# Kernel tuning notes

Hardware: AMD Instinct MI355X
Metric: run time of the kernel (lower is better)

Reference implementation:

```python
import jax, jax.numpy as jnp
import numpy as np

D = 256          # d_embed
KD = 256         # key_d_embed
NHEAD = 8
DK = D // NHEAD  # 32
QH = QW = 128
QWS = 16
KH = KW = 64
KWS = 8
R = QWS // KWS   # qk_ratio = 2
SCALE = 1.0 / np.sqrt(DK)


def _rel_index():
    # query coords on fine grid, key coords scaled up by ratio R
    qc = np.stack(np.meshgrid(np.arange(QWS), np.arange(QWS), indexing='ij'), -1).reshape(-1, 2)
    kc = np.stack(np.meshgrid(np.arange(KWS), np.arange(KWS), indexing='ij'), -1).reshape(-1, 2) * R
    rel = qc[:, None, :] - kc[None, :, :] + (QWS - R)  # values in [0, 2*QWS-R-1]
    return jnp.asarray(rel[..., 0] * (2 * QWS - R) + rel[..., 1])  # (QWS^2, KWS^2)


def _partition(t, ws):
    # (B, h, H, W, d) -> (B, h, H/ws, W/ws, ws*ws, d)
    B, h, H, W, d = t.shape
    t = t.reshape(B, h, H // ws, ws, W // ws, ws, d).transpose(0, 1, 2, 4, 3, 5, 6)
    return t.reshape(B, h, H // ws, W // ws, ws * ws, d)


def _merge(t, ws, H, W):
    # inverse of _partition
    B, h, nH, nW, _, d = t.shape
    t = t.reshape(B, h, nH, nW, ws, ws, d).transpose(0, 1, 2, 4, 3, 5, 6)
    return t.reshape(B, h, H, W, d)


def setup_inputs() -> dict:
    key = jax.random.key(0)
    ks = jax.random.split(key, 9)
    x = jax.random.normal(ks[0], (8, QH, QW, D), dtype=jnp.float32)
    z = jax.random.normal(ks[1], (8, KH, KW, KD), dtype=jnp.float32)
    mask = jax.random.randint(ks[2], (1, NHEAD, QH // QWS, QW // QWS, QWS * QWS, KWS * KWS), 0, 2) == 1
    Wq = jax.random.normal(ks[3], (D, D), dtype=jnp.float32) * 0.02
    bq = jnp.zeros((D,), dtype=jnp.float32)
    Wkv = jax.random.normal(ks[4], (KD, 2 * D), dtype=jnp.float32) * 0.02
    bkv = jnp.zeros((2 * D,), dtype=jnp.float32)
    Wo = jax.random.normal(ks[5], (D, D), dtype=jnp.float32) * 0.02
    bo = jnp.zeros((D,), dtype=jnp.float32)
    rel_table = jax.random.normal(ks[6], ((2 * QWS - R) ** 2, NHEAD), dtype=jnp.float32) * 0.02
    return {"x": x, "z": z, "mask": mask, "Wq": Wq, "bq": bq, "Wkv": Wkv, "bkv": bkv, "Wo": Wo, "bo": bo, "rel_table": rel_table}


def reference(x, z, mask, Wq, bq, Wkv, bkv, Wo, bo, rel_table):
    B, H, W, _ = x.shape
    q = (x @ Wq + bq).reshape(B, H, W, NHEAD, DK).transpose(0, 3, 1, 2, 4)        # (B,h,H,W,dk)
    kv = (z @ Wkv + bkv).reshape(B, KH, KW, 2, NHEAD, DK).transpose(3, 0, 4, 1, 2, 5)
    k, v = kv[0], kv[1]                                                           # (B,h,_H,_W,dk)
    sq, sk = QWS // 2, KWS // 2
    q = jnp.roll(q, (-sq, -sq), axis=(2, 3))
    k = jnp.roll(k, (-sk, -sk), axis=(2, 3))
    v = jnp.roll(v, (-sk, -sk), axis=(2, 3))
    q = _partition(q, QWS)   # (B,h,nh,nw,QWS^2,dk)
    k = _partition(k, KWS)   # (B,h,nh,nw,KWS^2,dk)
    v = _partition(v, KWS)
    attn = jnp.einsum('bhnmqd,bhnmkd->bhnmqk', q, k) * SCALE
    bias = rel_table[_rel_index()].transpose(2, 0, 1)[None, :, None, None]        # (1,h,1,1,QWS^2,KWS^2)
    attn = attn + bias
    attn = jnp.where(mask, jnp.float32(-1e9), attn)
    attn = jax.nn.softmax(attn, axis=-1)
    out = jnp.einsum('bhnmqk,bhnmkd->bhnmqd', attn, v)
    out = _merge(out, QWS, H, W)
    out = jnp.roll(out, (sq, sq), axis=(2, 3))
    out = out.transpose(0, 2, 3, 1, 4).reshape(B, H, W, D)
    return out @ Wo + bo
```

## Files before the change

kernel.cpp:

```cpp
#include <hip/hip_runtime.h>
#include <hip/hip_bf16.h>
#include <type_traits>


typedef __attribute__((ext_vector_type(8))) short short8v;
typedef __attribute__((ext_vector_type(4))) float f32x4;
typedef __attribute__((ext_vector_type(8))) unsigned short ushort8v;
typedef __attribute__((ext_vector_type(4))) unsigned short ushort4v;

#define DEV __device__ __forceinline__

DEV unsigned short f2bf(float f) {
    union { float f; unsigned u; } v; v.f = f;
    unsigned r = v.u + 0x7FFFu + ((v.u >> 16) & 1u);
    return (unsigned short)(r >> 16);
}

#define ATT_SCALE 0.17677669529663687f

__global__ void prep_weights(const float* __restrict__ Wq, const float* __restrict__ Wkv,
                             const float* __restrict__ Wo,
                             unsigned short* __restrict__ WqT, unsigned short* __restrict__ WkvT,
                             unsigned short* __restrict__ WoT) {
    int idx = blockIdx.x * 256 + threadIdx.x;
    if (idx < 65536) {
        int n = idx >> 8, k = idx & 255;
        WqT[idx] = f2bf(Wq[k * 256 + n] * ATT_SCALE);
    } else if (idx < 196608) {
        int i = idx - 65536;
        int n = i >> 8, k = i & 255;
        WkvT[i] = f2bf(Wkv[k * 512 + n]);
    } else {
        int i = idx - 196608;
        int n = i >> 8, k = i & 255;
        WoT[i] = f2bf(Wo[k * 256 + n]);
    }
}

__global__ void prep_bias(const float* __restrict__ rel_table, const float* __restrict__ bq,
                          float* __restrict__ biasb, float* __restrict__ bqs) {
    int idx = blockIdx.x * 256 + threadIdx.x;
    if (idx < 131072) {
        int head = idx >> 14;
        int q = (idx >> 6) & 255;
        int k = idx & 63;
        int qi = q >> 4, qj = q & 15;
        int ki = k >> 3, kj = k & 7;
        int r0 = qi - 2 * ki + 14, r1 = qj - 2 * kj + 14;
        biasb[idx] = rel_table[(r0 * 30 + r1) * 8 + head];
    } else if (idx < 131328) {
        int i = idx - 131072;
        bqs[i] = bq[i] * ATT_SCALE;
    }
}

__global__ void prep_mask(const int* __restrict__ mask, unsigned long long* __restrict__ mp) {
    int idx = blockIdx.x * 256 + threadIdx.x;
    const int4* src = reinterpret_cast<const int4*>(mask + (size_t)idx * 64);
    unsigned long long bits = 0;
#pragma unroll
    for (int c = 0; c < 16; ++c) {
        int4 v = src[c];
        if (v.x) bits |= 1ull << (c * 4 + 0);
        if (v.y) bits |= 1ull << (c * 4 + 1);
        if (v.z) bits |= 1ull << (c * 4 + 2);
        if (v.w) bits |= 1ull << (c * 4 + 3);
    }
    mp[idx] = bits;
}

template <typename InT, bool OUT_BF16>
__global__ __launch_bounds__(256) void gemm_proj(
    const InT* __restrict__ A, const unsigned short* __restrict__ BT,
    const float* __restrict__ bias, void* __restrict__ Cout,
    int M, int N, int K)
{
    __shared__ __align__(16) unsigned short As[128][40];
    __shared__ __align__(16) unsigned short Bs[128][40];

    const int tid = threadIdx.x;
    const int mb = blockIdx.y * 128;
    const int nb = blockIdx.x * 128;
    const int w = tid >> 6, lane = tid & 63, lr = lane & 15, lg = lane >> 4;
    const int wm = (w >> 1) * 64, wn = (w & 1) * 64;

    f32x4 acc[4][4];
#pragma unroll
    for (int i = 0; i < 4; ++i)
#pragma unroll
        for (int j = 0; j < 4; ++j) acc[i][j] = {0.f, 0.f, 0.f, 0.f};

    for (int kb = 0; kb < K; kb += 32) {
        if constexpr (std::is_same<InT, float>::value) {
#pragma unroll
            for (int i = 0; i < 4; ++i) {
                int row = (tid >> 3) + i * 32;
                int c4 = (tid & 7) * 4;
                const float4 v = *reinterpret_cast<const float4*>(
                    &A[(size_t)(mb + row) * K + kb + c4]);
                ushort4v u = { f2bf(v.x), f2bf(v.y), f2bf(v.z), f2bf(v.w) };
                *reinterpret_cast<ushort4v*>(&As[row][c4]) = u;
            }
        } else {
#pragma unroll
            for (int i = 0; i < 2; ++i) {
                int flat = tid + i * 256;
                int row = flat >> 2, c8 = (flat & 3) * 8;
                ushort8v v = *reinterpret_cast<const ushort8v*>(
                    &A[(size_t)(mb + row) * K + kb + c8]);
                *reinterpret_cast<ushort8v*>(&As[row][c8]) = v;
            }
        }
#pragma unroll
        for (int i = 0; i < 2; ++i) {
            int flat = tid + i * 256;
            int row = flat >> 2, c8 = (flat & 3) * 8;
            ushort8v v = *reinterpret_cast<const ushort8v*>(
                &BT[(size_t)(nb + row) * K + kb + c8]);
            *reinterpret_cast<ushort8v*>(&Bs[row][c8]) = v;
        }
        __syncthreads();

        short8v af[4], bfr[4];
#pragma unroll
        for (int mt = 0; mt < 4; ++mt)
            af[mt] = *reinterpret_cast<const short8v*>(&As[wm + mt * 16 + lr][lg * 8]);
#pragma unroll
        for (int nt = 0; nt < 4; ++nt)
            bfr[nt] = *reinterpret_cast<const short8v*>(&Bs[wn + nt * 16 + lr][lg * 8]);
#pragma unroll
        for (int mt = 0; mt < 4; ++mt)
#pragma unroll
            for (int nt = 0; nt < 4; ++nt)
                acc[mt][nt] = __builtin_amdgcn_mfma_f32_16x16x32_bf16(
                    af[mt], bfr[nt], acc[mt][nt], 0, 0, 0);
        __syncthreads();
    }

#pragma unroll
    for (int mt = 0; mt < 4; ++mt)
#pragma unroll
        for (int nt = 0; nt < 4; ++nt)
#pragma unroll
            for (int j = 0; j < 4; ++j) {
                int row = mb + wm + mt * 16 + lg * 4 + j;
                int col = nb + wn + nt * 16 + lr;
                float v = acc[mt][nt][j] + bias[col];
                if constexpr (OUT_BF16)
                    ((unsigned short*)Cout)[(size_t)row * N + col] = f2bf(v);
                else
                    ((float*)Cout)[(size_t)row * N + col] = v;
            }
}

__global__ __launch_bounds__(256) void win_attn(
    unsigned short* __restrict__ Qbuf,
    const unsigned short* __restrict__ KVbuf,
    const unsigned long long* __restrict__ maskp,
    const float* __restrict__ biasb)
{
    __shared__ __align__(16) unsigned char Pb[256 * 128];
    __shared__ __align__(16) unsigned short Vt[32][72];

    const int tid = threadIdx.x;
    const int win = blockIdx.x, head = blockIdx.y, b = blockIdx.z;
    const int wi = win >> 3, wj = win & 7;
    const int w = tid >> 6, lane = tid & 63, lr = lane & 15, lg = lane >> 4;
    const int qb = w * 64;

    {
        int key = tid & 63, c = tid >> 6;
        int kr = (wi * 8 + (key >> 3) + 4) & 63;
        int kc = (wj * 8 + (key & 7) + 4) & 63;
        ushort8v v = *reinterpret_cast<const ushort8v*>(
            KVbuf + ((size_t)(b * 4096 + kr * 64 + kc)) * 512 + 256 + head * 32 + c * 8);
#pragma unroll
        for (int e = 0; e < 8; ++e) Vt[c * 8 + e][key] = v[e];
    }

    short8v qf[4], kf[4];
#pragma unroll
    for (int mt = 0; mt < 4; ++mt) {
        int q = qb + mt * 16 + lr;
        int gr = (wi * 16 + (q >> 4) + 8) & 127;
        int gc = (wj * 16 + (q & 15) + 8) & 127;
        qf[mt] = *reinterpret_cast<const short8v*>(
            Qbuf + ((size_t)(b * 16384 + gr * 128 + gc)) * 256 + head * 32 + lg * 8);
    }
#pragma unroll
    for (int nt = 0; nt < 4; ++nt) {
        int key = nt * 16 + lr;
        int kr = (wi * 8 + (key >> 3) + 4) & 63;
        int kc = (wj * 8 + (key & 7) + 4) & 63;
        kf[nt] = *reinterpret_cast<const short8v*>(
            KVbuf + ((size_t)(b * 4096 + kr * 64 + kc)) * 512 + head * 32 + lg * 8);
    }

    f32x4 s[4][4];
#pragma unroll
    for (int mt = 0; mt < 4; ++mt)
#pragma unroll
        for (int nt = 0; nt < 4; ++nt) s[mt][nt] = {0.f, 0.f, 0.f, 0.f};
    __builtin_amdgcn_s_setprio(1);
#pragma unroll
    for (int mt = 0; mt < 4; ++mt)
#pragma unroll
        for (int nt = 0; nt < 4; ++nt)
            s[mt][nt] = __builtin_amdgcn_mfma_f32_16x16x32_bf16(qf[mt], kf[nt], s[mt][nt], 0, 0, 0);
    __builtin_amdgcn_s_setprio(0);

    const unsigned long long* mrow = maskp + (size_t)(head * 64 + win) * 256;
#pragma unroll
    for (int mt = 0; mt < 4; ++mt) {
#pragma unroll
        for (int j = 0; j < 4; ++j) {
            int q = qb + mt * 16 + lg * 4 + j;
            unsigned long long mb = mrow[q];
            const float* brow = biasb + (size_t)(head * 256 + q) * 64;
            float v[4];
            float m = -3.0e38f;
#pragma unroll
            for (int nt = 0; nt < 4; ++nt) {
                int key = nt * 16 + lr;
                float sv = s[mt][nt][j] + brow[key];
                if ((mb >> key) & 1ull) sv = -1.0e9f;
                v[nt] = sv;
                m = fmaxf(m, sv);
            }
#pragma unroll
            for (int d = 1; d < 16; d <<= 1) m = fmaxf(m, __shfl_xor(m, d, 64));
            float sum = 0.f;
#pragma unroll
            for (int nt = 0; nt < 4; ++nt) { v[nt] = __expf(v[nt] - m); sum += v[nt]; }
#pragma unroll
            for (int d = 1; d < 16; d <<= 1) sum += __shfl_xor(sum, d, 64);
            float inv = 1.0f / sum;
            int sw = (q & 7) << 4;
#pragma unroll
            for (int nt = 0; nt < 4; ++nt) {
                int off = q * 128 + (((nt * 16 + lr) * 2) ^ sw);
                *reinterpret_cast<unsigned short*>(Pb + off) = f2bf(v[nt] * inv);
            }
        }
    }

    __syncthreads();

    f32x4 o[4][2];
#pragma unroll
    for (int mt = 0; mt < 4; ++mt)
#pragma unroll
        for (int nt = 0; nt < 2; ++nt) o[mt][nt] = {0.f, 0.f, 0.f, 0.f};
#pragma unroll
    for (int kc = 0; kc < 2; ++kc) {
        short8v pf[4], vf[2];
#pragma unroll
        for (int mt = 0; mt < 4; ++mt) {
            int row = qb + mt * 16 + lr;
            int coff = (kc * 64 + lg * 16) ^ ((row & 7) << 4);
            pf[mt] = *reinterpret_cast<const short8v*>(Pb + row * 128 + coff);
        }
#pragma unroll
        for (int nt = 0; nt < 2; ++nt)
            vf[nt] = *reinterpret_cast<const short8v*>(&Vt[nt * 16 + lr][kc * 32 + lg * 8]);
        __builtin_amdgcn_s_setprio(1);
#pragma unroll
        for (int mt = 0; mt < 4; ++mt)
#pragma unroll
            for (int nt = 0; nt < 2; ++nt)
                o[mt][nt] = __builtin_amdgcn_mfma_f32_16x16x32_bf16(pf[mt], vf[nt], o[mt][nt], 0, 0, 0);
        __builtin_amdgcn_s_setprio(0);
    }

#pragma unroll
    for (int mt = 0; mt < 4; ++mt)
#pragma unroll
        for (int j = 0; j < 4; ++j) {
            int q = qb + mt * 16 + lg * 4 + j;
            int gr = (wi * 16 + (q >> 4) + 8) & 127;
            int gc = (wj * 16 + (q & 15) + 8) & 127;
            unsigned short* dst =
                Qbuf + ((size_t)(b * 16384 + gr * 128 + gc)) * 256 + head * 32;
#pragma unroll
            for (int nt = 0; nt < 2; ++nt)
                dst[nt * 16 + lr] = f2bf(o[mt][nt][j]);
        }
}

extern "C" void kernel_launch(void* const* d_in, const int* in_sizes, int n_in,
                              void* d_out, int out_size, void* d_ws, size_t ws_size,
                              hipStream_t stream) {
    const float* x    = (const float*)d_in[0];
    const float* z    = (const float*)d_in[1];
    const int*   mask = (const int*)d_in[2];
    const float* Wq   = (const float*)d_in[3];
    const float* bq   = (const float*)d_in[4];
    const float* Wkv  = (const float*)d_in[5];
    const float* bkv  = (const float*)d_in[6];
    const float* Wo   = (const float*)d_in[7];
    const float* bo   = (const float*)d_in[8];
    const float* rel  = (const float*)d_in[9];
    float* out = (float*)d_out;

    char* ws = (char*)d_ws;
    unsigned short*     Qbuf  = (unsigned short*)(ws);
    unsigned short*     KVbuf = (unsigned short*)(ws + 67108864);
    unsigned short*     WqT   = (unsigned short*)(ws + 100663296);
    unsigned short*     WkvT  = (unsigned short*)(ws + 100794368);
    unsigned short*     WoT   = (unsigned short*)(ws + 101056512);
    float*              biasb = (float*)(ws + 101187584);
    unsigned long long* maskp = (unsigned long long*)(ws + 101711872);
    float*              bqs   = (float*)(ws + 102760448);

    prep_weights<<<1024, 256, 0, stream>>>(Wq, Wkv, Wo, WqT, WkvT, WoT);
    prep_bias<<<513, 256, 0, stream>>>(rel, bq, biasb, bqs);
    prep_mask<<<512, 256, 0, stream>>>(mask, maskp);

    gemm_proj<float, true><<<dim3(2, 1024), 256, 0, stream>>>(
        x, WqT, bqs, (void*)Qbuf, 131072, 256, 256);
    gemm_proj<float, true><<<dim3(4, 256), 256, 0, stream>>>(
        z, WkvT, bkv, (void*)KVbuf, 32768, 512, 256);
    win_attn<<<dim3(64, 8, 8), 256, 0, stream>>>(Qbuf, KVbuf, maskp, biasb);
    gemm_proj<unsigned short, false><<<dim3(2, 1024), 256, 0, stream>>>(
        Qbuf, WoT, bo, (void*)out, 131072, 256, 256);
}
```

Measured before the change: 222.1 us.

## Double-buffer projection GEMM with direct global-to-LDS loads and swizzled LDS

Rewrites the projection GEMM main loop to double-buffer LDS tiles, prefetching the next K-slice while MFMAs run on the current one. Bf16 operands are staged with global_load_lds direct copies, while fp32 inputs are prefetched into registers and converted after the MFMAs. The padded LDS layout is replaced by an XOR-swizzled 64-byte row layout to avoid bank conflicts. The aim is to hide global memory latency and remove a barrier per iteration, at the cost of doubled LDS use and more register pressure.

```diff
diff --git a/kernel.cpp b/kernel.cpp
--- a/kernel.cpp
+++ b/kernel.cpp
@@ -69,72 +69,109 @@
     mp[idx] = bits;
 }
 
-template <typename InT, bool OUT_BF16>
+template <bool AF32, bool OUT_BF16>
 __global__ __launch_bounds__(256) void gemm_proj(
-    const InT* __restrict__ A, const unsigned short* __restrict__ BT,
+    const void* __restrict__ Ain, const unsigned short* __restrict__ BT,
     const float* __restrict__ bias, void* __restrict__ Cout,
     int M, int N, int K)
 {
-    __shared__ __align__(16) unsigned short As[128][40];
-    __shared__ __align__(16) unsigned short Bs[128][40];
+    __shared__ __align__(16) unsigned char As[2][8192];
+    __shared__ __align__(16) unsigned char Bs[2][8192];
+    const float* Af = (const float*)Ain;
+    const unsigned short* Ab = (const unsigned short*)Ain;
 
     const int tid = threadIdx.x;
-    const int mb = blockIdx.y * 128;
-    const int nb = blockIdx.x * 128;
+    const int mb = blockIdx.y * 128, nb = blockIdx.x * 128;
     const int w = tid >> 6, lane = tid & 63, lr = lane & 15, lg = lane >> 4;
     const int wm = (w >> 1) * 64, wn = (w & 1) * 64;
 
+    const int cr0 = (w << 5) + (lane >> 2);
+    const int csp = lane & 3;
+    const int cs0 = csp ^ ((cr0 >> 1) & 3);
+    const int cs1 = csp ^ (((cr0 + 16) >> 1) & 3);
+
+    auto stageB = [&](int buf, int kb) {
+        __builtin_amdgcn_global_load_lds(
+            (const __attribute__((address_space(1))) void*)(BT + (size_t)(nb + cr0) * K + kb + cs0 * 8),
+            (__attribute__((address_space(3))) void*)(&Bs[buf][w << 11]), 16, 0, 0);
+        __builtin_amdgcn_global_load_lds(
+            (const __attribute__((address_space(1))) void*)(BT + (size_t)(nb + cr0 + 16) * K + kb + cs1 * 8),
+            (__attribute__((address_space(3))) void*)(&Bs[buf][(w << 11) + 1024]), 16, 0, 0);
+    };
+    auto stageA_lds = [&](int buf, int kb) {
+        __builtin_amdgcn_global_load_lds(
+            (const __attribute__((address_space(1))) void*)(Ab + (size_t)(mb + cr0) * K + kb + cs0 * 8),
+            (__attribute__((address_space(3))) void*)(&As[buf][w << 11]), 16, 0, 0);
+        __builtin_amdgcn_global_load_lds(
+            (const __attribute__((address_space(1))) void*)(Ab + (size_t)(mb + cr0 + 16) * K + kb + cs1 * 8),
+            (__attribute__((address_space(3))) void*)(&As[buf][(w << 11) + 1024]), 16, 0, 0);
+    };
+
+    float4 areg[2][2];
+    auto loadA = [&](int kb) {
+#pragma unroll
+        for (int i = 0; i < 2; ++i) {
+            int flat = tid + (i << 8);
+            int r = flat >> 2, sp = flat & 3;
+            int s = sp ^ ((r >> 1) & 3);
+            const float* src = Af + (size_t)(mb + r) * K + kb + s * 8;
+            areg[i][0] = *reinterpret_cast<const float4*>(src);
+            areg[i][1] = *reinterpret_cast<const float4*>(src + 4);
+        }
+    };
+    auto writeA = [&](int buf) {
+#pragma unroll
+        for (int i = 0; i < 2; ++i) {
+            int flat = tid + (i << 8);
+            int r = flat >> 2, sp = flat & 3;
+            ushort8v u = { f2bf(areg[i][0].x), f2bf(areg[i][0].y),
+                           f2bf(areg[i][0].z), f2bf(areg[i][0].w),
+                           f2bf(areg[i][1].x), f2bf(areg[i][1].y),
+                           f2bf(areg[i][1].z), f2bf(areg[i][1].w) };
+            *reinterpret_cast<ushort8v*>(&As[buf][r * 64 + sp * 16]) = u;
+        }
+    };
+
+    auto rdA = [&](int buf, int row) -> short8v {
+        int swz = (lg ^ ((row >> 1) & 3)) << 4;
+        return *reinterpret_cast<const short8v*>(&As[buf][row * 64 + swz]);
+    };
+    auto rdB = [&](int buf, int row) -> short8v {
+        int swz = (lg ^ ((row >> 1) & 3)) << 4;
+        return *reinterpret_cast<const short8v*>(&Bs[buf][row * 64 + swz]);
+    };
+
     f32x4 acc[4][4];
 #pragma unroll
     for (int i = 0; i < 4; ++i)
 #pragma unroll
         for (int j = 0; j < 4; ++j) acc[i][j] = {0.f, 0.f, 0.f, 0.f};
 
-    for (int kb = 0; kb < K; kb += 32) {
-        if constexpr (std::is_same<InT, float>::value) {
-#pragma unroll
-            for (int i = 0; i < 4; ++i) {
-                int row = (tid >> 3) + i * 32;
-                int c4 = (tid & 7) * 4;
-                const float4 v = *reinterpret_cast<const float4*>(
-                    &A[(size_t)(mb + row) * K + kb + c4]);
-                ushort4v u = { f2bf(v.x), f2bf(v.y), f2bf(v.z), f2bf(v.w) };
-                *reinterpret_cast<ushort4v*>(&As[row][c4]) = u;
-            }
-        } else {
-#pragma unroll
-            for (int i = 0; i < 2; ++i) {
-                int flat = tid + i * 256;
-                int row = flat >> 2, c8 = (flat & 3) * 8;
-                ushort8v v = *reinterpret_cast<const ushort8v*>(
-                    &A[(size_t)(mb + row) * K + kb + c8]);
-                *reinterpret_cast<ushort8v*>(&As[row][c8]) = v;
-            }
-        }
-#pragma unroll
-        for (int i = 0; i < 2; ++i) {
-            int flat = tid + i * 256;
-            int row = flat >> 2, c8 = (flat & 3) * 8;
-            ushort8v v = *reinterpret_cast<const ushort8v*>(
-                &BT[(size_t)(nb + row) * K + kb + c8]);
-            *reinterpret_cast<ushort8v*>(&Bs[row][c8]) = v;
-        }
-        __syncthreads();
-
+    if constexpr (AF32) { loadA(0); stageB(0, 0); writeA(0); }
+    else               { stageA_lds(0, 0); stageB(0, 0); }
+    __syncthreads();
+
+    const int NT = K >> 5;
+    int cur = 0;
+    for (int t = 0; t < NT; ++t) {
+        if (t + 1 < NT) {
+            if constexpr (AF32) { loadA((t + 1) << 5); stageB(cur ^ 1, (t + 1) << 5); }
+            else { stageA_lds(cur ^ 1, (t + 1) << 5); stageB(cur ^ 1, (t + 1) << 5); }
+        }
         short8v af[4], bfr[4];
 #pragma unroll
-        for (int mt = 0; mt < 4; ++mt)
-            af[mt] = *reinterpret_cast<const short8v*>(&As[wm + mt * 16 + lr][lg * 8]);
-#pragma unroll
-        for (int nt = 0; nt < 4; ++nt)
-            bfr[nt] = *reinterpret_cast<const short8v*>(&Bs[wn + nt * 16 + lr][lg * 8]);
+        for (int mt = 0; mt < 4; ++mt) af[mt] = rdA(cur, wm + mt * 16 + lr);
+#pragma unroll
+        for (int nt = 0; nt < 4; ++nt) bfr[nt] = rdB(cur, wn + nt * 16 + lr);
 #pragma unroll
         for (int mt = 0; mt < 4; ++mt)
 #pragma unroll
             for (int nt = 0; nt < 4; ++nt)
                 acc[mt][nt] = __builtin_amdgcn_mfma_f32_16x16x32_bf16(
                     af[mt], bfr[nt], acc[mt][nt], 0, 0, 0);
+        if (t + 1 < NT) { if constexpr (AF32) writeA(cur ^ 1); }
         __syncthreads();
+        cur ^= 1;
     }
 
 #pragma unroll
@@ -316,11 +353,11 @@
     prep_bias<<<513, 256, 0, stream>>>(rel, bq, biasb, bqs);
     prep_mask<<<512, 256, 0, stream>>>(mask, maskp);
 
-    gemm_proj<float, true><<<dim3(2, 1024), 256, 0, stream>>>(
-        x, WqT, bqs, (void*)Qbuf, 131072, 256, 256);
-    gemm_proj<float, true><<<dim3(4, 256), 256, 0, stream>>>(
-        z, WkvT, bkv, (void*)KVbuf, 32768, 512, 256);
+    gemm_proj<true, true><<<dim3(2, 1024), 256, 0, stream>>>(
+        (const void*)x, WqT, bqs, (void*)Qbuf, 131072, 256, 256);
+    gemm_proj<true, true><<<dim3(4, 256), 256, 0, stream>>>(
+        (const void*)z, WkvT, bkv, (void*)KVbuf, 32768, 512, 256);
     win_attn<<<dim3(64, 8, 8), 256, 0, stream>>>(Qbuf, KVbuf, maskp, biasb);
-    gemm_proj<unsigned short, false><<<dim3(2, 1024), 256, 0, stream>>>(
-        Qbuf, WoT, bo, (void*)out, 131072, 256, 256);
-}
+    gemm_proj<false, false><<<dim3(2, 1024), 256, 0, stream>>>(
+        (const void*)Qbuf, WoT, bo, (void*)out, 131072, 256, 256);
+}
```

Measured after the change: 221.3 us. Within noise of the previous version (-0.4%).

## Stream A operands from global into registers with B fully resident in LDS

Applied to the files above, without the earlier changes.

Replaces the tiled projection GEMM with a kernel that loads the whole 128x256 bf16 B slice into swizzled LDS once. Each wave then streams its A rows straight from global memory into MFMA fragments, double-buffered in registers and converted from fp32 with packed bf16 intrinsics. Blocks grow to 512 threads covering 256 rows, which removes the per-k-step A staging through LDS and the barriers. The cost is 64KB of LDS per block and heavier register use, which may reduce occupancy.

```diff
diff --git a/kernel.cpp b/kernel.cpp
--- a/kernel.cpp
+++ b/kernel.cpp
@@ -14,6 +14,15 @@
     union { float f; unsigned u; } v; v.f = f;
     unsigned r = v.u + 0x7FFFu + ((v.u >> 16) & 1u);
     return (unsigned short)(r >> 16);
+}
+
+DEV short8v cvt_f32x8(const float4 lo, const float4 hi) {
+    union U { __hip_bfloat162 h[4]; short8v s; } u;
+    u.h[0] = __float22bfloat162_rn(float2{lo.x, lo.y});
+    u.h[1] = __float22bfloat162_rn(float2{lo.z, lo.w});
+    u.h[2] = __float22bfloat162_rn(float2{hi.x, hi.y});
+    u.h[3] = __float22bfloat162_rn(float2{hi.z, hi.w});
+    return u.s;
 }
 
 #define ATT_SCALE 0.17677669529663687f
@@ -69,20 +78,45 @@
     mp[idx] = bits;
 }
 
-template <typename InT, bool OUT_BF16>
-__global__ __launch_bounds__(256) void gemm_proj(
-    const InT* __restrict__ A, const unsigned short* __restrict__ BT,
+template <bool AF32, bool OUT_BF16>
+__global__ __launch_bounds__(512) void gemm_stream(
+    const void* __restrict__ Ain, const unsigned short* __restrict__ BT,
     const float* __restrict__ bias, void* __restrict__ Cout,
-    int M, int N, int K)
+    int M, int N)
 {
-    __shared__ __align__(16) unsigned short As[128][40];
-    __shared__ __align__(16) unsigned short Bs[128][40];
+    __shared__ __align__(16) unsigned char Bs[65536];
+    const float* Af = (const float*)Ain;
+    const unsigned short* Ab = (const unsigned short*)Ain;
 
     const int tid = threadIdx.x;
-    const int mb = blockIdx.y * 128;
-    const int nb = blockIdx.x * 128;
     const int w = tid >> 6, lane = tid & 63, lr = lane & 15, lg = lane >> 4;
-    const int wm = (w >> 1) * 64, wn = (w & 1) * 64;
+    const int mb = blockIdx.x * 256;
+    const int nb = blockIdx.y * 128;
+    const int wm = (w >> 1) * 64;
+    const int wn = (w & 1) * 64;
+
+    {
+        int row = tid >> 2, part = tid & 3;
+        const unsigned short* src = BT + (size_t)(nb + row) * 256 + part * 64;
+        int rsw = (row >> 1) & 3;
+        ushort8v bv[8];
+#pragma unroll
+        for (int i = 0; i < 8; ++i)
+            bv[i] = *reinterpret_cast<const ushort8v*>(src + i * 8);
+#pragma unroll
+        for (int h = 0; h < 2; ++h)
+#pragma unroll
+            for (int sl = 0; sl < 4; ++sl)
+                *reinterpret_cast<ushort8v*>(
+                    &Bs[(part * 2 + h) * 8192 + row * 64 + ((sl ^ rsw) << 4)]) = bv[h * 4 + sl];
+    }
+    __syncthreads();
+
+    const int swzB = (lg ^ ((lr >> 1) & 3)) << 4;
+    auto rdB = [&](int kt, int nt) -> short8v {
+        return *reinterpret_cast<const short8v*>(
+            &Bs[kt * 8192 + (wn + nt * 16 + lr) * 64 + swzB]);
+    };
 
     f32x4 acc[4][4];
 #pragma unroll
@@ -90,51 +124,65 @@
 #pragma unroll
         for (int j = 0; j < 4; ++j) acc[i][j] = {0.f, 0.f, 0.f, 0.f};
 
-    for (int kb = 0; kb < K; kb += 32) {
-        if constexpr (std::is_same<InT, float>::value) {
-#pragma unroll
-            for (int i = 0; i < 4; ++i) {
-                int row = (tid >> 3) + i * 32;
-                int c4 = (tid & 7) * 4;
-                const float4 v = *reinterpret_cast<const float4*>(
-                    &A[(size_t)(mb + row) * K + kb + c4]);
-                ushort4v u = { f2bf(v.x), f2bf(v.y), f2bf(v.z), f2bf(v.w) };
-                *reinterpret_cast<ushort4v*>(&As[row][c4]) = u;
+    if constexpr (AF32) {
+        const float* Abase = Af + (size_t)(mb + wm + lr) * 256 + lg * 8;
+        float4 aP[4][2], aQ[4][2];
+        auto loadA = [&](float4 (&buf)[4][2], int kt) {
+#pragma unroll
+            for (int mt = 0; mt < 4; ++mt) {
+                const float* p = Abase + mt * 4096 + kt * 32;
+                buf[mt][0] = *reinterpret_cast<const float4*>(p);
+                buf[mt][1] = *reinterpret_cast<const float4*>(p + 4);
             }
-        } else {
-#pragma unroll
-            for (int i = 0; i < 2; ++i) {
-                int flat = tid + i * 256;
-                int row = flat >> 2, c8 = (flat & 3) * 8;
-                ushort8v v = *reinterpret_cast<const ushort8v*>(
-                    &A[(size_t)(mb + row) * K + kb + c8]);
-                *reinterpret_cast<ushort8v*>(&As[row][c8]) = v;
-            }
-        }
-#pragma unroll
-        for (int i = 0; i < 2; ++i) {
-            int flat = tid + i * 256;
-            int row = flat >> 2, c8 = (flat & 3) * 8;
-            ushort8v v = *reinterpret_cast<const ushort8v*>(
-                &BT[(size_t)(nb + row) * K + kb + c8]);
-            *reinterpret_cast<ushort8v*>(&Bs[row][c8]) = v;
-        }
-        __syncthreads();
-
-        short8v af[4], bfr[4];
-#pragma unroll
-        for (int mt = 0; mt < 4; ++mt)
-            af[mt] = *reinterpret_cast<const short8v*>(&As[wm + mt * 16 + lr][lg * 8]);
-#pragma unroll
-        for (int nt = 0; nt < 4; ++nt)
-            bfr[nt] = *reinterpret_cast<const short8v*>(&Bs[wn + nt * 16 + lr][lg * 8]);
-#pragma unroll
-        for (int mt = 0; mt < 4; ++mt)
-#pragma unroll
-            for (int nt = 0; nt < 4; ++nt)
-                acc[mt][nt] = __builtin_amdgcn_mfma_f32_16x16x32_bf16(
-                    af[mt], bfr[nt], acc[mt][nt], 0, 0, 0);
-        __syncthreads();
+        };
+        auto compute = [&](float4 (&buf)[4][2], int kt) {
+            short8v af[4], bf[4];
+#pragma unroll
+            for (int mt = 0; mt < 4; ++mt) af[mt] = cvt_f32x8(buf[mt][0], buf[mt][1]);
+#pragma unroll
+            for (int nt = 0; nt < 4; ++nt) bf[nt] = rdB(kt, nt);
+#pragma unroll
+            for (int mt = 0; mt < 4; ++mt)
+#pragma unroll
+                for (int nt = 0; nt < 4; ++nt)
+                    acc[mt][nt] = __builtin_amdgcn_mfma_f32_16x16x32_bf16(
+                        af[mt], bf[nt], acc[mt][nt], 0, 0, 0);
+        };
+        loadA(aP, 0);
+#pragma unroll
+        for (int kk = 0; kk < 8; kk += 2) {
+            if (kk + 1 < 8) loadA(aQ, kk + 1);
+            compute(aP, kk);
+            if (kk + 2 < 8) loadA(aP, kk + 2);
+            compute(aQ, kk + 1);
+        }
+    } else {
+        const unsigned short* Abase = Ab + (size_t)(mb + wm + lr) * 256 + lg * 8;
+        short8v aP[4], aQ[4];
+        auto loadA = [&](short8v (&buf)[4], int kt) {
+#pragma unroll
+            for (int mt = 0; mt < 4; ++mt)
+                buf[mt] = *reinterpret_cast<const short8v*>(Abase + mt * 4096 + kt * 32);
+        };
+        auto compute = [&](short8v (&buf)[4], int kt) {
+            short8v bf[4];
+#pragma unroll
+            for (int nt = 0; nt < 4; ++nt) bf[nt] = rdB(kt, nt);
+#pragma unroll
+            for (int mt = 0; mt < 4; ++mt)
+#pragma unroll
+                for (int nt = 0; nt < 4; ++nt)
+                    acc[mt][nt] = __builtin_amdgcn_mfma_f32_16x16x32_bf16(
+                        buf[mt], bf[nt], acc[mt][nt], 0, 0, 0);
+        };
+        loadA(aP, 0);
+#pragma unroll
+        for (int kk = 0; kk < 8; kk += 2) {
+            if (kk + 1 < 8) loadA(aQ, kk + 1);
+            compute(aP, kk);
+            if (kk + 2 < 8) loadA(aP, kk + 2);
+            compute(aQ, kk + 1);
+        }
     }
 
 #pragma unroll
@@ -316,11 +364,11 @@
     prep_bias<<<513, 256, 0, stream>>>(rel, bq, biasb, bqs);
     prep_mask<<<512, 256, 0, stream>>>(mask, maskp);
 
-    gemm_proj<float, true><<<dim3(2, 1024), 256, 0, stream>>>(
-        x, WqT, bqs, (void*)Qbuf, 131072, 256, 256);
-    gemm_proj<float, true><<<dim3(4, 256), 256, 0, stream>>>(
-        z, WkvT, bkv, (void*)KVbuf, 32768, 512, 256);
+    gemm_stream<true, true><<<dim3(512, 2), 512, 0, stream>>>(
+        (const void*)x, WqT, bqs, (void*)Qbuf, 131072, 256);
+    gemm_stream<true, true><<<dim3(128, 4), 512, 0, stream>>>(
+        (const void*)z, WkvT, bkv, (void*)KVbuf, 32768, 512);
     win_attn<<<dim3(64, 8, 8), 256, 0, stream>>>(Qbuf, KVbuf, maskp, biasb);
-    gemm_proj<unsigned short, false><<<dim3(2, 1024), 256, 0, stream>>>(
-        Qbuf, WoT, bo, (void*)out, 131072, 256, 256);
-}
+    gemm_stream<false, false><<<dim3(512, 2), 512, 0, stream>>>(
+        (const void*)Qbuf, WoT, bo, (void*)out, 131072, 256);
+}
```

Result: slower. 272.3 us (+22.6%).

## Restructure projection GEMMs to keep full-K weight tile in LDS and stream A from registers

Applied to the files above, without the earlier changes.

Replaces the tiled 128x128 GEMM with a kernel that loads the entire K=256 slice of a 64-column weight tile into swizzled LDS once. Each wave then streams its A rows straight from global memory into registers, double-buffered, and converts fp32 to bf16 in registers. This removes the per-K-step A staging through shared memory and the paired barriers, and uses a 128x64 tile that doubles the grid. The cost is that A is read from global memory several times (once per N-block) without LDS reuse, and K is hardcoded to 256.

```diff
diff --git a/kernel.cpp b/kernel.cpp
--- a/kernel.cpp
+++ b/kernel.cpp
@@ -14,6 +14,15 @@
     union { float f; unsigned u; } v; v.f = f;
     unsigned r = v.u + 0x7FFFu + ((v.u >> 16) & 1u);
     return (unsigned short)(r >> 16);
+}
+
+DEV short8v cvt_f32x8(const float4 lo, const float4 hi) {
+    union U { __hip_bfloat162 h[4]; short8v s; } u;
+    u.h[0] = __float22bfloat162_rn(float2{lo.x, lo.y});
+    u.h[1] = __float22bfloat162_rn(float2{lo.z, lo.w});
+    u.h[2] = __float22bfloat162_rn(float2{hi.x, hi.y});
+    u.h[3] = __float22bfloat162_rn(float2{hi.z, hi.w});
+    return u.s;
 }
 
 #define ATT_SCALE 0.17677669529663687f
@@ -69,82 +78,120 @@
     mp[idx] = bits;
 }
 
-template <typename InT, bool OUT_BF16>
-__global__ __launch_bounds__(256) void gemm_proj(
-    const InT* __restrict__ A, const unsigned short* __restrict__ BT,
+template <bool AF32, bool OUT_BF16>
+__global__ __launch_bounds__(256) void gemm_v5(
+    const void* __restrict__ Ain, const unsigned short* __restrict__ BT,
     const float* __restrict__ bias, void* __restrict__ Cout,
-    int M, int N, int K)
+    int M, int N)
 {
-    __shared__ __align__(16) unsigned short As[128][40];
-    __shared__ __align__(16) unsigned short Bs[128][40];
+    __shared__ __align__(16) unsigned char Bs[32768];
+    const float* Af = (const float*)Ain;
+    const unsigned short* Ab = (const unsigned short*)Ain;
 
     const int tid = threadIdx.x;
+    const int w = tid >> 6, lane = tid & 63, lr = lane & 15, lg = lane >> 4;
+    const int nb = blockIdx.x * 64;
     const int mb = blockIdx.y * 128;
-    const int nb = blockIdx.x * 128;
-    const int w = tid >> 6, lane = tid & 63, lr = lane & 15, lg = lane >> 4;
-    const int wm = (w >> 1) * 64, wn = (w & 1) * 64;
-
-    f32x4 acc[4][4];
-#pragma unroll
-    for (int i = 0; i < 4; ++i)
+    const int wm = mb + w * 32;
+
+    {
+        int r = tid >> 2, p = tid & 3;
+        const unsigned short* src = BT + (size_t)(nb + r) * 256 + p * 64;
+        int rsw = (r >> 1) & 3;
+#pragma unroll
+        for (int h = 0; h < 2; ++h) {
+            int kt = p * 2 + h;
+#pragma unroll
+            for (int sl = 0; sl < 4; ++sl) {
+                ushort8v v = *reinterpret_cast<const ushort8v*>(src + h * 32 + sl * 8);
+                *reinterpret_cast<ushort8v*>(
+                    &Bs[kt * 4096 + r * 64 + ((sl ^ rsw) << 4)]) = v;
+            }
+        }
+    }
+    __syncthreads();
+
+    const int swz = (lg ^ ((lr >> 1) & 3)) << 4;
+
+    f32x4 acc[2][4];
+#pragma unroll
+    for (int i = 0; i < 2; ++i)
 #pragma unroll
         for (int j = 0; j < 4; ++j) acc[i][j] = {0.f, 0.f, 0.f, 0.f};
 
-    for (int kb = 0; kb < K; kb += 32) {
-        if constexpr (std::is_same<InT, float>::value) {
-#pragma unroll
-            for (int i = 0; i < 4; ++i) {
-                int row = (tid >> 3) + i * 32;
-                int c4 = (tid & 7) * 4;
-                const float4 v = *reinterpret_cast<const float4*>(
-                    &A[(size_t)(mb + row) * K + kb + c4]);
-                ushort4v u = { f2bf(v.x), f2bf(v.y), f2bf(v.z), f2bf(v.w) };
-                *reinterpret_cast<ushort4v*>(&As[row][c4]) = u;
-            }
-        } else {
-#pragma unroll
-            for (int i = 0; i < 2; ++i) {
-                int flat = tid + i * 256;
-                int row = flat >> 2, c8 = (flat & 3) * 8;
-                ushort8v v = *reinterpret_cast<const ushort8v*>(
-                    &A[(size_t)(mb + row) * K + kb + c8]);
-                *reinterpret_cast<ushort8v*>(&As[row][c8]) = v;
-            }
-        }
-#pragma unroll
-        for (int i = 0; i < 2; ++i) {
-            int flat = tid + i * 256;
-            int row = flat >> 2, c8 = (flat & 3) * 8;
-            ushort8v v = *reinterpret_cast<const ushort8v*>(
-                &BT[(size_t)(nb + row) * K + kb + c8]);
-            *reinterpret_cast<ushort8v*>(&Bs[row][c8]) = v;
-        }
-        __syncthreads();
-
-        short8v af[4], bfr[4];
-#pragma unroll
-        for (int mt = 0; mt < 4; ++mt)
-            af[mt] = *reinterpret_cast<const short8v*>(&As[wm + mt * 16 + lr][lg * 8]);
+    if constexpr (AF32) {
+        const float* A0 = Af + (size_t)(wm + lr) * 256 + lg * 8;
+        const float* A1 = Af + (size_t)(wm + 16 + lr) * 256 + lg * 8;
+        float4 p00, p01, p10, p11, q00, q01, q10, q11;
+
+#define LD_P(kt) { p00 = *reinterpret_cast<const float4*>(A0 + (kt) * 32);     \
+                   p01 = *reinterpret_cast<const float4*>(A0 + (kt) * 32 + 4); \
+                   p10 = *reinterpret_cast<const float4*>(A1 + (kt) * 32);     \
+                   p11 = *reinterpret_cast<const float4*>(A1 + (kt) * 32 + 4); }
+#define LD_Q(kt) { q00 = *reinterpret_cast<const float4*>(A0 + (kt) * 32);     \
+                   q01 = *reinterpret_cast<const float4*>(A0 + (kt) * 32 + 4); \
+                   q10 = *reinterpret_cast<const float4*>(A1 + (kt) * 32);     \
+                   q11 = *reinterpret_cast<const float4*>(A1 + (kt) * 32 + 4); }
+#define STEP(x00, x01, x10, x11, kt) {                                          \
+        short8v a0 = cvt_f32x8(x00, x01), a1 = cvt_f32x8(x10, x11);             \
+        _Pragma("unroll")                                                       \
+        for (int nt = 0; nt < 4; ++nt) {                                        \
+            short8v bf = *reinterpret_cast<const short8v*>(                     \
+                &Bs[(kt) * 4096 + (nt * 16 + lr) * 64 + swz]);                  \
+            acc[0][nt] = __builtin_amdgcn_mfma_f32_16x16x32_bf16(a0, bf, acc[0][nt], 0, 0, 0); \
+            acc[1][nt] = __builtin_amdgcn_mfma_f32_16x16x32_bf16(a1, bf, acc[1][nt], 0, 0, 0); \
+        } }
+
+        LD_P(0);
+#pragma unroll
+        for (int kk = 0; kk < 8; kk += 2) {
+            if (kk + 1 < 8) LD_Q(kk + 1);
+            STEP(p00, p01, p10, p11, kk);
+            if (kk + 2 < 8) LD_P(kk + 2);
+            if (kk + 1 < 8) STEP(q00, q01, q10, q11, kk + 1);
+        }
+#undef LD_P
+#undef LD_Q
+#undef STEP
+    } else {
+        const unsigned short* A0 = Ab + (size_t)(wm + lr) * 256 + lg * 8;
+        const unsigned short* A1 = Ab + (size_t)(wm + 16 + lr) * 256 + lg * 8;
+        short8v p0, p1, q0, q1;
+
+#define LD_P(kt) { p0 = *reinterpret_cast<const short8v*>(A0 + (kt) * 32);  \
+                   p1 = *reinterpret_cast<const short8v*>(A1 + (kt) * 32); }
+#define LD_Q(kt) { q0 = *reinterpret_cast<const short8v*>(A0 + (kt) * 32);  \
+                   q1 = *reinterpret_cast<const short8v*>(A1 + (kt) * 32); }
+#define STEP(x0, x1, kt) {                                                      \
+        _Pragma("unroll")                                                       \
+        for (int nt = 0; nt < 4; ++nt) {                                        \
+            short8v bf = *reinterpret_cast<const short8v*>(                     \
+                &Bs[(kt) * 4096 + (nt * 16 + lr) * 64 + swz]);                  \
+            acc[0][nt] = __builtin_amdgcn_mfma_f32_16x16x32_bf16(x0, bf, acc[0][nt], 0, 0, 0); \
+            acc[1][nt] = __builtin_amdgcn_mfma_f32_16x16x32_bf16(x1, bf, acc[1][nt], 0, 0, 0); \
+        } }
+
+        LD_P(0);
+#pragma unroll
+        for (int kk = 0; kk < 8; kk += 2) {
+            if (kk + 1 < 8) LD_Q(kk + 1);
+            STEP(p0, p1, kk);
+            if (kk + 2 < 8) LD_P(kk + 2);
+            if (kk + 1 < 8) STEP(q0, q1, kk + 1);
+        }
+#undef LD_P
+#undef LD_Q
+#undef STEP
+    }
+
+#pragma unroll
+    for (int mt = 0; mt < 2; ++mt)
 #pragma unroll
         for (int nt = 0; nt < 4; ++nt)
-            bfr[nt] = *reinterpret_cast<const short8v*>(&Bs[wn + nt * 16 + lr][lg * 8]);
-#pragma unroll
-        for (int mt = 0; mt < 4; ++mt)
-#pragma unroll
-            for (int nt = 0; nt < 4; ++nt)
-                acc[mt][nt] = __builtin_amdgcn_mfma_f32_16x16x32_bf16(
-                    af[mt], bfr[nt], acc[mt][nt], 0, 0, 0);
-        __syncthreads();
-    }
-
-#pragma unroll
-    for (int mt = 0; mt < 4; ++mt)
-#pragma unroll
-        for (int nt = 0; nt < 4; ++nt)
 #pragma unroll
             for (int j = 0; j < 4; ++j) {
-                int row = mb + wm + mt * 16 + lg * 4 + j;
-                int col = nb + wn + nt * 16 + lr;
+                int row = wm + mt * 16 + lg * 4 + j;
+                int col = nb + nt * 16 + lr;
                 float v = acc[mt][nt][j] + bias[col];
                 if constexpr (OUT_BF16)
                     ((unsigned short*)Cout)[(size_t)row * N + col] = f2bf(v);
@@ -316,11 +363,11 @@
     prep_bias<<<513, 256, 0, stream>>>(rel, bq, biasb, bqs);
     prep_mask<<<512, 256, 0, stream>>>(mask, maskp);
 
-    gemm_proj<float, true><<<dim3(2, 1024), 256, 0, stream>>>(
-        x, WqT, bqs, (void*)Qbuf, 131072, 256, 256);
-    gemm_proj<float, true><<<dim3(4, 256), 256, 0, stream>>>(
-        z, WkvT, bkv, (void*)KVbuf, 32768, 512, 256);
+    gemm_v5<true, true><<<dim3(4, 1024), 256, 0, stream>>>(
+        (const void*)x, WqT, bqs, (void*)Qbuf, 131072, 256);
+    gemm_v5<true, true><<<dim3(8, 256), 256, 0, stream>>>(
+        (const void*)z, WkvT, bkv, (void*)KVbuf, 32768, 512);
     win_attn<<<dim3(64, 8, 8), 256, 0, stream>>>(Qbuf, KVbuf, maskp, biasb);
-    gemm_proj<unsigned short, false><<<dim3(2, 1024), 256, 0, stream>>>(
-        Qbuf, WoT, bo, (void*)out, 131072, 256, 256);
-}
+    gemm_v5<false, false><<<dim3(4, 1024), 256, 0, stream>>>(
+        (const void*)Qbuf, WoT, bo, (void*)out, 131072, 256);
+}
```

New measurement: 289.8 us. 1.3x slower.
